# Kernel tuning notes

Hardware: AMD Instinct MI355X
Metric: run time of the kernel (lower is better)

## Reference

```python
import jax, jax.numpy as jnp
import numpy as np

DIM = 128          # per-stream channels (init arg `dim`)
C = 2 * DIM        # fused channels
NH = 8             # num_heads
HD = C // NH       # head_dim = 32
K = 3              # kernel_size
DIL = (2, 3)       # dilation list
ND = len(DIL)
SCALE = HD ** -0.5


def setup_inputs() -> dict:
    key = jax.random.key(0)
    ks = jax.random.split(key, 4)
    B, H, W = 4, 80, 80
    rgb = jax.random.normal(ks[0], (B, DIM, H, W), jnp.float32)
    ir = jax.random.normal(ks[1], (B, DIM, H, W), jnp.float32)
    w_qkv = jax.random.normal(ks[2], (3 * C, C), jnp.float32) * (C ** -0.5)
    w_proj = jax.random.normal(ks[3], (C, C), jnp.float32) * (C ** -0.5)
    b_proj = jnp.zeros((C,), jnp.float32)
    return {"rgb": rgb, "ir": ir, "w_qkv": w_qkv, "w_proj": w_proj, "b_proj": b_proj}


def _unfold(x, k, d):
    # nn.Unfold(k, dilation=d, padding=d*(k-1)//2, stride=1) -> [B, c, k*k, H, W]
    B, c, H, W = x.shape
    p = d * (k - 1) // 2
    xp = jnp.pad(x, ((0, 0), (0, 0), (p, p), (p, p)))
    pats = [xp[:, :, i * d:i * d + H, j * d:j * d + W]
            for i in range(k) for j in range(k)]
    return jnp.stack(pats, axis=2)


def _dilate_attention(q, k, v, d):
    # q,k,v: [B, c, H, W] with c = C // ND; attention over k*k dilated neighborhood
    B, c, H, W = q.shape
    h = c // HD
    N = H * W
    qr = q.reshape(B, h, HD, N)                      # [B,h,hd,N]
    ku = _unfold(k, K, d).reshape(B, h, HD, K * K, N)  # [B,h,hd,K2,N]
    vu = _unfold(v, K, d).reshape(B, h, HD, K * K, N)
    attn = jnp.einsum('bhdn,bhdkn->bhnk', qr, ku) * SCALE   # [B,h,N,K2]
    attn = jax.nn.softmax(attn, axis=-1)
    out = jnp.einsum('bhnk,bhdkn->bnhd', attn, vu)          # head-major channels
    return out.reshape(B, H, W, c)


def reference(rgb, ir, w_qkv, w_proj, b_proj):
    y = jnp.concatenate([rgb, ir], axis=1)            # [B, C, H, W]
    B, Cc, H, W = y.shape
    # 1x1 conv qkv, then split channels as [3, num_dilation, C//num_dilation]
    qkv = jnp.einsum('bchw,oc->bohw', y, w_qkv).reshape(B, 3, ND, Cc // ND, H, W)
    outs = [_dilate_attention(qkv[:, 0, i], qkv[:, 1, i], qkv[:, 2, i], DIL[i])
            for i in range(ND)]
    x = jnp.concatenate(outs, axis=-1)                # [B, H, W, C], dilation-major
    x = x @ w_proj.T + b_proj                         # proj Linear(C, C)
    # residual: add rgb to first half of channels, ir to second half
    return x + y.transpose(0, 2, 3, 1)
```

## Files before the change

### kernel.cpp

```cpp
#include <hip/hip_runtime.h>

#define HH 80
#define WW 80
#define NPIX 6400
#define NB 4
#define BN 25600
#define CDIM 256
#define QKVC 768
#define SCALE 0.17677669529663689f

typedef __attribute__((ext_vector_type(8))) short short8;
typedef __attribute__((ext_vector_type(4))) float floatx4;

__device__ __forceinline__ float b2f(ushort u) {
    return __uint_as_float(((uint)u) << 16);
}
__device__ __forceinline__ ushort f2b(float f) {
    uint u = __float_as_uint(f);
    return (ushort)((u + 0x7fffu + ((u >> 16) & 1u)) >> 16);
}
__device__ __forceinline__ void unpack8(uint4 v, float* f) {
    f[0] = __uint_as_float(v.x << 16); f[1] = __uint_as_float(v.x & 0xffff0000u);
    f[2] = __uint_as_float(v.y << 16); f[3] = __uint_as_float(v.y & 0xffff0000u);
    f[4] = __uint_as_float(v.z << 16); f[5] = __uint_as_float(v.z & 0xffff0000u);
    f[6] = __uint_as_float(v.w << 16); f[7] = __uint_as_float(v.w & 0xffff0000u);
}
__device__ __forceinline__ void gload_lds16(const void* gptr, void* lptr) {
    __builtin_amdgcn_global_load_lds(
        (const __attribute__((address_space(1))) unsigned int*)gptr,
        (__attribute__((address_space(3))) unsigned int*)lptr,
        16, 0, 0);
}

__global__ __launch_bounds__(256) void cast_all_k(
    const float* __restrict__ rgb, const float* __restrict__ ir,
    const float* __restrict__ wq, const float* __restrict__ wp,
    ushort* __restrict__ Yb, ushort* __restrict__ wqb, ushort* __restrict__ wpb)
{
    const int tid = threadIdx.x;
    if (blockIdx.x >= 100) {
        int i = (((blockIdx.x - 100) * 8 + blockIdx.y) * 4 + blockIdx.z) * 256 + tid;
        if (i < QKVC * CDIM) wqb[i] = f2b(wq[i]);
        else                 wpb[i - QKVC * CDIM] = f2b(wp[i - QKVC * CDIM]);
        return;
    }
    __shared__ ushort T[32][72];
    const int pix0 = blockIdx.x * 64;
    const int cb = blockIdx.y;
    const int b = blockIdx.z;

    const int pl = tid & 63, cg = tid >> 6;
    #pragma unroll
    for (int cc = 0; cc < 32; cc += 4) {
        int c = cb * 32 + cc + cg;
        const float* src = (c < 128) ? (rgb + ((size_t)b * 128 + c) * NPIX)
                                     : (ir + ((size_t)b * 128 + (c - 128)) * NPIX);
        T[cc + cg][pl] = f2b(src[pix0 + pl]);
    }
    __syncthreads();
    const int nl = tid >> 2, c0 = (tid & 3) * 8;
    ushort tmp[8];
    #pragma unroll
    for (int j = 0; j < 8; ++j) tmp[j] = T[c0 + j][nl];
    uint4 v;
    v.x = tmp[0] | ((uint)tmp[1] << 16);
    v.y = tmp[2] | ((uint)tmp[3] << 16);
    v.z = tmp[4] | ((uint)tmp[5] << 16);
    v.w = tmp[6] | ((uint)tmp[7] << 16);
    *(uint4*)(&Yb[((size_t)(b * NPIX + pix0 + nl)) * CDIM + cb * 32 + c0]) = v;
}

__device__ __forceinline__ void gemm_nt_body64(
    const ushort* __restrict__ A, const ushort* __restrict__ W,
    ushort* As, ushort* Bs, int n0, int o0, floatx4 acc[4][4])
{
    const int tid = threadIdx.x;
    const int lane = tid & 63;
    const int wave = tid >> 6;
    const int wr = wave >> 1, wc = wave & 1;
    const int l15 = lane & 15, quad = lane >> 4;

    const int srow8 = tid >> 3;
    const int scol  = ((tid & 7) * 8) ^ ((srow8 & 1) << 5);
    const int par   = l15 & 1;

    for (int k0 = 0; k0 < CDIM; k0 += 64) {
        #pragma unroll
        for (int r = 0; r < 4; ++r) {
            const int row = r * 32 + srow8;
            gload_lds16(&A[(size_t)(n0 + row) * CDIM + k0 + scol],
                        As + r * 2048 + wave * 512);
            gload_lds16(&W[(size_t)(o0 + row) * CDIM + k0 + scol],
                        Bs + r * 2048 + wave * 512);
        }
        __syncthreads();
        #pragma unroll
        for (int s = 0; s < 2; ++s) {
            const int fc = ((s ^ par) << 5) + quad * 8;
            short8 af[4], bfr[4];
            #pragma unroll
            for (int i = 0; i < 4; ++i)
                af[i] = *(const short8*)(&As[(wr * 64 + i * 16 + l15) * 64 + fc]);
            #pragma unroll
            for (int j = 0; j < 4; ++j)
                bfr[j] = *(const short8*)(&Bs[(wc * 64 + j * 16 + l15) * 64 + fc]);
            #pragma unroll
            for (int i = 0; i < 4; ++i)
                #pragma unroll
                for (int j = 0; j < 4; ++j)
                    acc[i][j] = __builtin_amdgcn_mfma_f32_16x16x32_bf16(
                        bfr[j], af[i], acc[i][j], 0, 0, 0);
        }
        __syncthreads();
    }
}

__global__ __launch_bounds__(256) void gemm_qkv_mfma(
    const ushort* __restrict__ Yb, const ushort* __restrict__ Wb,
    ushort* __restrict__ qkv2)
{
    __shared__ __align__(16) ushort As[128 * 64];
    __shared__ __align__(16) ushort Bs[128 * 64];
    const int tid = threadIdx.x;
    const int lane = tid & 63;
    const int wave = tid >> 6;
    const int wr = wave >> 1, wc = wave & 1;
    const int l15 = lane & 15, quad = lane >> 4;

    const int bid = blockIdx.x;
    const int swz = (bid & 7) * 150 + (bid >> 3);
    const int n0 = (swz / 6) * 128;
    const int o0 = (swz % 6) * 128;

    floatx4 acc[4][4] = {};
    gemm_nt_body64(Yb, Wb, As, Bs, n0, o0, acc);

    #pragma unroll
    for (int i = 0; i < 4; ++i) {
        const int n = n0 + wr * 64 + i * 16 + l15;
        #pragma unroll
        for (int j = 0; j < 4; ++j) {
            const int o4 = o0 + wc * 64 + j * 16 + quad * 4;
            uint2 v;
            v.x = f2b(acc[i][j][0]) | ((uint)f2b(acc[i][j][1]) << 16);
            v.y = f2b(acc[i][j][2]) | ((uint)f2b(acc[i][j][3]) << 16);
            *(uint2*)(qkv2 + (size_t)(o4 >> 5) * BN * 32 + (size_t)n * 32 + (o4 & 31)) = v;
        }
    }
}

template<int D, bool EDGE>
__device__ __forceinline__ void attn_phase(
    const ushort* __restrict__ qkv2, ushort* Xl,
    int b, int dh, int y0, int x0, int px)
{
    const int py = px >> 3, pxx = px & 7;
    const int yy0 = y0 + py, xx0 = x0 + pxx;
    const int n = b * NPIX + yy0 * WW + xx0;
    const ushort* Qc = qkv2 + (size_t)dh * BN * 32;
    const ushort* Kc = qkv2 + (size_t)(8 + dh) * BN * 32;
    const ushort* Vc = qkv2 + (size_t)(16 + dh) * BN * 32;

    float q[32];
    {
        const uint4* qp = (const uint4*)(Qc + (size_t)n * 32);
        uint4 v0 = qp[0], v1 = qp[1], v2 = qp[2], v3 = qp[3];
        unpack8(v0, q); unpack8(v1, q + 8); unpack8(v2, q + 16); unpack8(v3, q + 24);
    }

    float sc[9];
    #pragma unroll
    for (int t = 0; t < 9; ++t) {
        const int dy = t / 3 - 1, dx = t % 3 - 1;
        int yy = yy0 + dy * D, xx = xx0 + dx * D;
        bool ok = true;
        if (EDGE) {
            ok = (yy >= 0 && yy < HH && xx >= 0 && xx < WW);
            yy = min(max(yy, 0), HH - 1);
            xx = min(max(xx, 0), WW - 1);
        }
        const uint4* kp = (const uint4*)(Kc + (size_t)(b * NPIX + yy * WW + xx) * 32);
        uint4 k0 = kp[0], k1 = kp[1], k2 = kp[2], k3 = kp[3];
        float kv[32];
        unpack8(k0, kv); unpack8(k1, kv + 8); unpack8(k2, kv + 16); unpack8(k3, kv + 24);
        float s = 0.f;
        #pragma unroll
        for (int j = 0; j < 32; ++j) s += q[j] * kv[j];
        sc[t] = (EDGE && !ok) ? 0.f : s * SCALE;
    }

    float m = sc[0];
    #pragma unroll
    for (int t = 1; t < 9; ++t) m = fmaxf(m, sc[t]);
    float sum = 0.f;
    #pragma unroll
    for (int t = 0; t < 9; ++t) { sc[t] = __expf(sc[t] - m); sum += sc[t]; }
    const float inv = 1.f / sum;

    float o[32];
    #pragma unroll
    for (int j = 0; j < 32; ++j) o[j] = 0.f;
    #pragma unroll
    for (int t = 0; t < 9; ++t) {
        const int dy = t / 3 - 1, dx = t % 3 - 1;
        int yy = yy0 + dy * D, xx = xx0 + dx * D;
        bool ok = true;
        if (EDGE) {
            ok = (yy >= 0 && yy < HH && xx >= 0 && xx < WW);
            yy = min(max(yy, 0), HH - 1);
            xx = min(max(xx, 0), WW - 1);
        }
        const uint4* vp = (const uint4*)(Vc + (size_t)(b * NPIX + yy * WW + xx) * 32);
        uint4 v0 = vp[0], v1 = vp[1], v2 = vp[2], v3 = vp[3];
        float vv[32];
        unpack8(v0, vv); unpack8(v1, vv + 8); unpack8(v2, vv + 16); unpack8(v3, vv + 24);
        const float wgt = (EDGE && !ok) ? 0.f : sc[t] * inv;
        #pragma unroll
        for (int j = 0; j < 32; ++j) o[j] += wgt * vv[j];
    }

    #pragma unroll
    for (int m4 = 0; m4 < 4; ++m4) {
        uint4 v;
        v.x = f2b(o[8 * m4 + 0]) | ((uint)f2b(o[8 * m4 + 1]) << 16);
        v.y = f2b(o[8 * m4 + 2]) | ((uint)f2b(o[8 * m4 + 3]) << 16);
        v.z = f2b(o[8 * m4 + 4]) | ((uint)f2b(o[8 * m4 + 5]) << 16);
        v.w = f2b(o[8 * m4 + 6]) | ((uint)f2b(o[8 * m4 + 7]) << 16);
        const int slot = (dh * 4 + m4) ^ (px & 7);
        *(uint4*)(&Xl[px * 256 + slot * 8]) = v;
    }
}

__global__ __launch_bounds__(256) void attn_proj_k(
    const ushort* __restrict__ qkv2, const ushort* __restrict__ Wpb,
    const float* __restrict__ bp, const ushort* __restrict__ Yb,
    float* __restrict__ out)
{
    __shared__ __align__(16) ushort Xl[32 * 256];
    __shared__ __align__(16) ushort Bs[256 * 64];
    const int tid = threadIdx.x;
    const int bid = blockIdx.x;
    const int swz = (bid & 7) * 100 + (bid >> 3);
    const int b  = swz / 200;
    const int t  = swz % 200;
    const int y0 = (t / 10) * 4, x0 = (t % 10) * 8;
    const bool inter = (y0 >= 4 && y0 <= 72 && x0 >= 8 && x0 <= 64);

    const int px = tid & 31;
    const int dh = tid >> 5;

    if (dh < 4) {
        if (inter) attn_phase<2, false>(qkv2, Xl, b, dh, y0, x0, px);
        else       attn_phase<2, true >(qkv2, Xl, b, dh, y0, x0, px);
    } else {
        if (inter) attn_phase<3, false>(qkv2, Xl, b, dh, y0, x0, px);
        else       attn_phase<3, true >(qkv2, Xl, b, dh, y0, x0, px);
    }
    __syncthreads();

    const int lane = tid & 63;
    const int wave = tid >> 6;
    const int l15 = lane & 15, quad = lane >> 4;
    const int srow8 = tid >> 3;
    const int scol  = ((tid & 7) * 8) ^ ((srow8 & 1) << 5);
    const int par   = l15 & 1;

    floatx4 acc[2][4] = {};
    for (int k0 = 0; k0 < CDIM; k0 += 64) {
        #pragma unroll
        for (int r = 0; r < 8; ++r) {
            const int row = r * 32 + srow8;
            gload_lds16(&Wpb[(size_t)row * CDIM + k0 + scol],
                        Bs + r * 2048 + wave * 512);
        }
        __syncthreads();
        #pragma unroll
        for (int s = 0; s < 2; ++s) {
            const int fc = ((s ^ par) << 5) + quad * 8;
            short8 af[2], bfr[4];
            #pragma unroll
            for (int i = 0; i < 2; ++i) {
                const int row = i * 16 + l15;
                const int slot = ((k0 >> 3) + s * 4 + quad) ^ (row & 7);
                af[i] = *(const short8*)(&Xl[row * 256 + slot * 8]);
            }
            #pragma unroll
            for (int j = 0; j < 4; ++j)
                bfr[j] = *(const short8*)(&Bs[(wave * 64 + j * 16 + l15) * 64 + fc]);
            #pragma unroll
            for (int i = 0; i < 2; ++i)
                #pragma unroll
                for (int j = 0; j < 4; ++j)
                    acc[i][j] = __builtin_amdgcn_mfma_f32_16x16x32_bf16(
                        bfr[j], af[i], acc[i][j], 0, 0, 0);
        }
        __syncthreads();
    }

    #pragma unroll
    for (int i = 0; i < 2; ++i) {
        const int r15 = i * 16 + l15;
        const int n = b * NPIX + (y0 + (r15 >> 3)) * WW + (x0 + (r15 & 7));
        #pragma unroll
        for (int j = 0; j < 4; ++j) {
            const int o4 = wave * 64 + j * 16 + quad * 4;
            const float4 bias = *(const float4*)(bp + o4);
            const ushort4 res = *(const ushort4*)(Yb + (size_t)n * CDIM + o4);
            float4 v;
            v.x = acc[i][j][0] + bias.x + b2f(res.x);
            v.y = acc[i][j][1] + bias.y + b2f(res.y);
            v.z = acc[i][j][2] + bias.z + b2f(res.z);
            v.w = acc[i][j][3] + bias.w + b2f(res.w);
            *(float4*)(out + (size_t)n * CDIM + o4) = v;
        }
    }
}

extern "C" void kernel_launch(void* const* d_in, const int* in_sizes, int n_in,
                              void* d_out, int out_size, void* d_ws, size_t ws_size,
                              hipStream_t stream) {
    const float* rgb    = (const float*)d_in[0];
    const float* ir     = (const float*)d_in[1];
    const float* w_qkv  = (const float*)d_in[2];
    const float* w_proj = (const float*)d_in[3];
    const float* b_proj = (const float*)d_in[4];
    float* out = (float*)d_out;

    ushort* qkv2 = (ushort*)d_ws;
    ushort* Yb   = qkv2 + (size_t)24 * BN * 32;
    ushort* Wqb  = Yb + (size_t)BN * CDIM;
    ushort* Wpb  = Wqb + (size_t)QKVC * CDIM;

    cast_all_k<<<dim3(132, 8, NB), 256, 0, stream>>>(rgb, ir, w_qkv, w_proj,
                                                     Yb, Wqb, Wpb);
    gemm_qkv_mfma<<<dim3(1200), 256, 0, stream>>>(Yb, Wqb, qkv2);
    attn_proj_k<<<dim3(800), 256, 0, stream>>>(qkv2, Wpb, b_proj, Yb, out);
}
```

Before: 137.9 us.

## Fuse fp32 cast and transpose into QKV GEMM, read residual from fp32 inputs

Removes the separate cast kernel. The QKV GEMM now loads fp32 rgb/ir activations and weights straight into registers, converts them to bf16 and writes them into swizzled LDS, with a register prefetch of the next k-tile. The proj epilogue reads the residual directly from the fp32 NCHW inputs instead of a bf16 copy, which also makes the residual exact. This saves one launch and the Yb/Wqb round trip. The cost is per-block redundant conversion of weights and activations, and scalar strided residual reads in the epilogue.

```diff
diff --git a/kernel.cpp b/kernel.cpp
--- a/kernel.cpp
+++ b/kernel.cpp
@@ -32,68 +32,82 @@
         16, 0, 0);
 }
 
-__global__ __launch_bounds__(256) void cast_all_k(
+__global__ __launch_bounds__(256) void qkv_fused_k(
     const float* __restrict__ rgb, const float* __restrict__ ir,
     const float* __restrict__ wq, const float* __restrict__ wp,
-    ushort* __restrict__ Yb, ushort* __restrict__ wqb, ushort* __restrict__ wpb)
+    ushort* __restrict__ qkv2, ushort* __restrict__ wpb)
 {
     const int tid = threadIdx.x;
-    if (blockIdx.x >= 100) {
-        int i = (((blockIdx.x - 100) * 8 + blockIdx.y) * 4 + blockIdx.z) * 256 + tid;
-        if (i < QKVC * CDIM) wqb[i] = f2b(wq[i]);
-        else                 wpb[i - QKVC * CDIM] = f2b(wp[i - QKVC * CDIM]);
+    if (blockIdx.x >= 1200) {
+        const int t0 = (blockIdx.x - 1200) * 256 + tid;
+        #pragma unroll
+        for (int g = 0; g < 32; ++g) {
+            const int i4 = g * 512 + t0;
+            const float4 v = ((const float4*)wp)[i4];
+            ushort4 o4;
+            o4.x = f2b(v.x); o4.y = f2b(v.y); o4.z = f2b(v.z); o4.w = f2b(v.w);
+            ((ushort4*)wpb)[i4] = o4;
+        }
         return;
     }
-    __shared__ ushort T[32][72];
-    const int pix0 = blockIdx.x * 64;
-    const int cb = blockIdx.y;
-    const int b = blockIdx.z;
-
-    const int pl = tid & 63, cg = tid >> 6;
-    #pragma unroll
-    for (int cc = 0; cc < 32; cc += 4) {
-        int c = cb * 32 + cc + cg;
-        const float* src = (c < 128) ? (rgb + ((size_t)b * 128 + c) * NPIX)
-                                     : (ir + ((size_t)b * 128 + (c - 128)) * NPIX);
-        T[cc + cg][pl] = f2b(src[pix0 + pl]);
-    }
-    __syncthreads();
-    const int nl = tid >> 2, c0 = (tid & 3) * 8;
-    ushort tmp[8];
-    #pragma unroll
-    for (int j = 0; j < 8; ++j) tmp[j] = T[c0 + j][nl];
-    uint4 v;
-    v.x = tmp[0] | ((uint)tmp[1] << 16);
-    v.y = tmp[2] | ((uint)tmp[3] << 16);
-    v.z = tmp[4] | ((uint)tmp[5] << 16);
-    v.w = tmp[6] | ((uint)tmp[7] << 16);
-    *(uint4*)(&Yb[((size_t)(b * NPIX + pix0 + nl)) * CDIM + cb * 32 + c0]) = v;
-}
-
-__device__ __forceinline__ void gemm_nt_body64(
-    const ushort* __restrict__ A, const ushort* __restrict__ W,
-    ushort* As, ushort* Bs, int n0, int o0, floatx4 acc[4][4])
-{
-    const int tid = threadIdx.x;
+
+    __shared__ __align__(16) ushort As[128 * 64];
+    __shared__ __align__(16) ushort Bs[128 * 64];
+
     const int lane = tid & 63;
     const int wave = tid >> 6;
     const int wr = wave >> 1, wc = wave & 1;
     const int l15 = lane & 15, quad = lane >> 4;
-
-    const int srow8 = tid >> 3;
-    const int scol  = ((tid & 7) * 8) ^ ((srow8 & 1) << 5);
-    const int par   = l15 & 1;
-
-    for (int k0 = 0; k0 < CDIM; k0 += 64) {
-        #pragma unroll
-        for (int r = 0; r < 4; ++r) {
-            const int row = r * 32 + srow8;
-            gload_lds16(&A[(size_t)(n0 + row) * CDIM + k0 + scol],
-                        As + r * 2048 + wave * 512);
-            gload_lds16(&W[(size_t)(o0 + row) * CDIM + k0 + scol],
-                        Bs + r * 2048 + wave * 512);
+    const int par = l15 & 1;
+
+    const int bid = blockIdx.x;
+    const int swz = (bid & 7) * 150 + (bid >> 3);
+    const int n0 = (swz / 6) * 128;
+    const int o0 = (swz % 6) * 128;
+    const int b = n0 / NPIX;
+    const int pix0 = n0 - b * NPIX;
+
+    const int c2 = (tid & 31) * 2;
+    const int pg = tid >> 5;
+
+    float a0f[16], a1f[16], w0f[16], w1f[16];
+
+    auto load_tile = [&](int k0) {
+        const float* asrc = (k0 < 128)
+            ? rgb + (size_t)(b * 128 + k0 + c2) * NPIX
+            : ir  + (size_t)(b * 128 + (k0 - 128) + c2) * NPIX;
+        const float* a0 = asrc + pix0 + pg * 16;
+        const float* a1 = a0 + NPIX;
+        #pragma unroll
+        for (int q = 0; q < 4; ++q) {
+            float4 v0 = ((const float4*)a0)[q];
+            float4 v1 = ((const float4*)a1)[q];
+            a0f[4*q+0] = v0.x; a0f[4*q+1] = v0.y; a0f[4*q+2] = v0.z; a0f[4*q+3] = v0.w;
+            a1f[4*q+0] = v1.x; a1f[4*q+1] = v1.y; a1f[4*q+2] = v1.z; a1f[4*q+3] = v1.w;
+        }
+        const float* wsrc = wq + (size_t)(o0 + pg * 16) * CDIM + k0 + c2;
+        #pragma unroll
+        for (int r = 0; r < 16; ++r) {
+            float2 v = *(const float2*)(wsrc + (size_t)r * CDIM);
+            w0f[r] = v.x; w1f[r] = v.y;
+        }
+    };
+
+    floatx4 acc[4][4] = {};
+    load_tile(0);
+
+    for (int t = 0; t < 4; ++t) {
+        #pragma unroll
+        for (int p = 0; p < 16; ++p) {
+            const int row = pg * 16 + p;
+            const int col = c2 ^ ((p & 1) << 5);
+            *(uint*)&As[row * 64 + col] =
+                (uint)f2b(a0f[p]) | ((uint)f2b(a1f[p]) << 16);
+            *(uint*)&Bs[row * 64 + col] =
+                (uint)f2b(w0f[p]) | ((uint)f2b(w1f[p]) << 16);
         }
         __syncthreads();
+        if (t < 3) load_tile((t + 1) * 64);
         #pragma unroll
         for (int s = 0; s < 2; ++s) {
             const int fc = ((s ^ par) << 5) + quad * 8;
@@ -113,27 +127,6 @@
         }
         __syncthreads();
     }
-}
-
-__global__ __launch_bounds__(256) void gemm_qkv_mfma(
-    const ushort* __restrict__ Yb, const ushort* __restrict__ Wb,
-    ushort* __restrict__ qkv2)
-{
-    __shared__ __align__(16) ushort As[128 * 64];
-    __shared__ __align__(16) ushort Bs[128 * 64];
-    const int tid = threadIdx.x;
-    const int lane = tid & 63;
-    const int wave = tid >> 6;
-    const int wr = wave >> 1, wc = wave & 1;
-    const int l15 = lane & 15, quad = lane >> 4;
-
-    const int bid = blockIdx.x;
-    const int swz = (bid & 7) * 150 + (bid >> 3);
-    const int n0 = (swz / 6) * 128;
-    const int o0 = (swz % 6) * 128;
-
-    floatx4 acc[4][4] = {};
-    gemm_nt_body64(Yb, Wb, As, Bs, n0, o0, acc);
 
     #pragma unroll
     for (int i = 0; i < 4; ++i) {
@@ -233,7 +226,8 @@
 
 __global__ __launch_bounds__(256) void attn_proj_k(
     const ushort* __restrict__ qkv2, const ushort* __restrict__ Wpb,
-    const float* __restrict__ bp, const ushort* __restrict__ Yb,
+    const float* __restrict__ bp,
+    const float* __restrict__ rgb, const float* __restrict__ ir,
     float* __restrict__ out)
 {
     __shared__ __align__(16) ushort Xl[32 * 256];
@@ -300,17 +294,20 @@
     #pragma unroll
     for (int i = 0; i < 2; ++i) {
         const int r15 = i * 16 + l15;
-        const int n = b * NPIX + (y0 + (r15 >> 3)) * WW + (x0 + (r15 & 7));
+        const int pixn = (y0 + (r15 >> 3)) * WW + (x0 + (r15 & 7));
+        const int n = b * NPIX + pixn;
         #pragma unroll
         for (int j = 0; j < 4; ++j) {
             const int o4 = wave * 64 + j * 16 + quad * 4;
             const float4 bias = *(const float4*)(bp + o4);
-            const ushort4 res = *(const ushort4*)(Yb + (size_t)n * CDIM + o4);
+            const float* rs = ((o4 < 128)
+                ? rgb + (size_t)(b * 128 + o4) * NPIX
+                : ir  + (size_t)(b * 128 + (o4 - 128)) * NPIX) + pixn;
             float4 v;
-            v.x = acc[i][j][0] + bias.x + b2f(res.x);
-            v.y = acc[i][j][1] + bias.y + b2f(res.y);
-            v.z = acc[i][j][2] + bias.z + b2f(res.z);
-            v.w = acc[i][j][3] + bias.w + b2f(res.w);
+            v.x = acc[i][j][0] + bias.x + rs[0];
+            v.y = acc[i][j][1] + bias.y + rs[NPIX];
+            v.z = acc[i][j][2] + bias.z + rs[2 * NPIX];
+            v.w = acc[i][j][3] + bias.w + rs[3 * NPIX];
             *(float4*)(out + (size_t)n * CDIM + o4) = v;
         }
     }
@@ -327,12 +324,9 @@
     float* out = (float*)d_out;
 
     ushort* qkv2 = (ushort*)d_ws;
-    ushort* Yb   = qkv2 + (size_t)24 * BN * 32;
-    ushort* Wqb  = Yb + (size_t)BN * CDIM;
-    ushort* Wpb  = Wqb + (size_t)QKVC * CDIM;
-
-    cast_all_k<<<dim3(132, 8, NB), 256, 0, stream>>>(rgb, ir, w_qkv, w_proj,
-                                                     Yb, Wqb, Wpb);
-    gemm_qkv_mfma<<<dim3(1200), 256, 0, stream>>>(Yb, Wqb, qkv2);
-    attn_proj_k<<<dim3(800), 256, 0, stream>>>(qkv2, Wpb, b_proj, Yb, out);
-}
+    ushort* Wpb  = qkv2 + (size_t)24 * BN * 32;
+
+    qkv_fused_k<<<dim3(1202), 256, 0, stream>>>(rgb, ir, w_qkv, w_proj,
+                                                qkv2, Wpb);
+    attn_proj_k<<<dim3(800), 256, 0, stream>>>(qkv2, Wpb, b_proj, rgb, ir, out);
+}
```

Result: slower. 155.3 us (+12.6%).
